# Performance work log

Measured on AMD Instinct MI355X. Metric: run time of the kernel, lower is better.

Reference implementation:

```python
import jax, jax.numpy as jnp
import numpy as np

DK = 128
B, S = 16, 2048

def setup_inputs() -> dict:
    key = jax.random.key(0)
    kq, kk, kv = jax.random.split(key, 3)
    q = jax.random.normal(kq, (B, S, DK), dtype=jnp.float32)
    k = jax.random.normal(kk, (B, S, DK), dtype=jnp.float32)
    v = jax.random.normal(kv, (B, S, DK), dtype=jnp.float32)
    return {"q": q, "k": k, "v": v}

def reference(q, k, v):
    # scores: [B, S, S]
    scale = 1.0 / jnp.sqrt(jnp.float32(DK))
    scores = jnp.einsum("bqd,bkd->bqk", q, k) * scale
    probs = jax.nn.softmax(scores, axis=-1)
    # dropout is identity in eval mode (training=None)
    return jnp.einsum("bqk,bkd->bqd", probs, v)
```

## Files before the change

### kernel.cpp

```cpp
#include <hip/hip_runtime.h>
#include <hip/hip_bf16.h>

#define BATCH 16
#define SEQ   2048
#define DK    128
#define NT    (SEQ / 2 / 32)
#define SC2   0.12751744f
#define THRL2 11.541560f

typedef __attribute__((ext_vector_type(8))) short short8v;
typedef __attribute__((ext_vector_type(4))) float float4v;

typedef const __attribute__((address_space(1))) unsigned int* gas_t;
typedef __attribute__((address_space(3))) unsigned int* las_t;

__device__ inline void gl_lds16(const void* g, void* l) {
    __builtin_amdgcn_global_load_lds((gas_t)g, (las_t)l, 16, 0, 0);
}

__device__ inline short f2bf(float f) {
    __hip_bfloat16 h = __float2bfloat16(f);
    unsigned short u;
    __builtin_memcpy(&u, &h, sizeof(u));
    return (short)u;
}

__device__ inline unsigned cvt_pk_bf16(float a, float b) {
    unsigned r;
    asm("v_cvt_pk_bf16_f32 %0, %1, %2" : "=v"(r) : "v"(a), "v"(b));
    return r;
}

__global__ __launch_bounds__(256)
void conv_k_kernel(const float* __restrict__ k, short* __restrict__ kb)
{
    size_t i = ((size_t)blockIdx.x * 256 + threadIdx.x) * 8;
    float4 a = *reinterpret_cast<const float4*>(k + i);
    float4 b = *reinterpret_cast<const float4*>(k + i + 4);
    short8v t;
    t[0] = f2bf(a.x * SC2); t[1] = f2bf(a.y * SC2); t[2] = f2bf(a.z * SC2); t[3] = f2bf(a.w * SC2);
    t[4] = f2bf(b.x * SC2); t[5] = f2bf(b.y * SC2); t[6] = f2bf(b.z * SC2); t[7] = f2bf(b.w * SC2);
    *reinterpret_cast<short8v*>(kb + i) = t;
}

__global__ __launch_bounds__(256)
void transpose_v_kernel(const float* __restrict__ v, short* __restrict__ vt)
{
    __shared__ float tile[32][33];
    const int tx = threadIdx.x & 31;
    const int ty = threadIdx.x >> 5;
    const int b  = blockIdx.z;
    const int s0 = blockIdx.x * 32;
    const int d0 = blockIdx.y * 32;

    const float* vb = v + ((size_t)b * SEQ + s0) * DK + d0;
#pragma unroll
    for (int i = 0; i < 4; ++i) {
        int r = ty + 8 * i;
        tile[r][tx] = vb[(size_t)r * DK + tx];
    }
    __syncthreads();

    const int s   = s0 + tx;
    const int kvl = s & 31;
    const int pos = (((kvl >> 2) & 3) << 3) | (((kvl >> 4) & 1) << 2) | (kvl & 3);
    const size_t col = (size_t)(s & ~31) | pos;

    short* vtb = vt + ((size_t)b * DK + d0) * SEQ;
#pragma unroll
    for (int i = 0; i < 4; ++i) {
        int r = ty + 8 * i;
        vtb[(size_t)r * SEQ + col] = f2bf(tile[tx][r]);
    }
}

__global__ __launch_bounds__(512)
void attn_fwd_v5(const float* __restrict__ q,
                 const short* __restrict__ kb,
                 const short* __restrict__ vt,
                 float* __restrict__ out)
{
    __shared__ __align__(16) char lds[65536];

    const int tid  = threadIdx.x;
    const int lane = tid & 63;
    const int wave = tid >> 6;
    const int qt   = wave & 3;
    const int h    = wave >> 2;
    const int b    = blockIdx.y;
    const int q0   = blockIdx.x * 64 + qt * 16;

    const int row  = lane & 15;
    const int grp  = lane >> 4;
    const int kswz = (row & 7) << 4;
    const int vswz = ((row >> 1) & 3) << 4;

    const float* qb = q + ((size_t)b * SEQ + q0) * DK;
    short8v qf[4];
#pragma unroll
    for (int c = 0; c < 4; ++c) {
        const float* p = qb + row * DK + c * 32 + grp * 8;
        float4 x = *reinterpret_cast<const float4*>(p);
        float4 y = *reinterpret_cast<const float4*>(p + 4);
        union { unsigned u[4]; short8v v; } pk;
        pk.u[0] = cvt_pk_bf16(x.x, x.y);
        pk.u[1] = cvt_pk_bf16(x.z, x.w);
        pk.u[2] = cvt_pk_bf16(y.x, y.y);
        pk.u[3] = cvt_pk_bf16(y.z, y.w);
        qf[c] = pk.v;
    }

    const char* kB = (const char*)(kb + (size_t)b * SEQ * DK);
    const char* vB = (const char*)(vt + (size_t)b * DK * SEQ);

    const char* src0[4];
    int         sstr[4];
    int         dsto[4];
#pragma unroll
    for (int i = 0; i < 4; ++i) {
        const int c = wave * 4 + i;
        if (c < 16) {
            const int hh = c >> 3, cc = c & 7;
            const int kr = 4 * cc + (lane >> 4);
            src0[i] = kB + (size_t)(hh * 1024 + kr) * 256
                         + (((lane & 15) << 4) ^ ((kr & 7) << 4));
            sstr[i] = 32 * 256;
            dsto[i] = hh * 8192 + cc * 1024;
        } else {
            const int hh = (c >> 3) & 1, cc = c & 7;
            const int vd = 16 * cc + (lane >> 2);
            src0[i] = vB + (size_t)vd * 4096 + hh * 2048
                         + (((lane & 3) << 4) ^ (((lane >> 3) & 3) << 4));
            sstr[i] = 32 * 2;
            dsto[i] = 16384 + hh * 8192 + cc * 1024;
        }
    }

    float m_run = -1e30f;
    float l_run = 0.0f;
    float4v o[8];
#pragma unroll
    for (int i = 0; i < 8; ++i) { o[i][0] = 0.f; o[i][1] = 0.f; o[i][2] = 0.f; o[i][3] = 0.f; }

    auto STAGE = [&](int bufsel, int t) {
        char* base = lds + bufsel * 32768;
#pragma unroll
        for (int i = 0; i < 4; ++i)
            gl_lds16(src0[i] + (size_t)t * sstr[i], base + dsto[i]);
    };

    STAGE(0, 0);
    __syncthreads();

    int buf = 0;
    for (int t = 0; t < NT; ++t) {
        if (t + 1 < NT) STAGE(buf ^ 1, t + 1);

        const char* Kl = lds + buf * 32768 + h * 8192;
        const char* Vl = lds + buf * 32768 + 16384 + h * 8192;

        float4v s[2];
        __builtin_amdgcn_s_setprio(1);
#pragma unroll
        for (int sub = 0; sub < 2; ++sub) {
            s[sub][0] = 0.f; s[sub][1] = 0.f; s[sub][2] = 0.f; s[sub][3] = 0.f;
            const char* kr = Kl + (sub * 16 + row) * 256;
#pragma unroll
            for (int c = 0; c < 4; ++c) {
                short8v kf = *reinterpret_cast<const short8v*>(kr + (((c << 6) | (grp << 4)) ^ kswz));
                s[sub] = __builtin_amdgcn_mfma_f32_16x16x32_bf16(kf, qf[c], s[sub], 0, 0, 0);
            }
        }
        __builtin_amdgcn_s_setprio(0);

        float mx = fmaxf(fmaxf(fmaxf(s[0][0], s[0][1]), fmaxf(s[0][2], s[0][3])),
                         fmaxf(fmaxf(s[1][0], s[1][1]), fmaxf(s[1][2], s[1][3])));
        mx = fmaxf(mx, __shfl_xor(mx, 16));
        mx = fmaxf(mx, __shfl_xor(mx, 32));

        if (!__all(mx <= m_run + THRL2)) {
            const float mnew  = fmaxf(m_run, mx);
            const float alpha = exp2f(m_run - mnew);
            l_run *= alpha;
            m_run = mnew;
            float aq[4];
#pragma unroll
            for (int r = 0; r < 4; ++r) aq[r] = __shfl(alpha, grp * 4 + r);
#pragma unroll
            for (int dblk = 0; dblk < 8; ++dblk)
#pragma unroll
                for (int r = 0; r < 4; ++r) o[dblk][r] *= aq[r];
        }

        float tsum = 0.f;
#pragma unroll
        for (int sub = 0; sub < 2; ++sub)
#pragma unroll
            for (int r = 0; r < 4; ++r) {
                const float e = exp2f(s[sub][r] - m_run);
                s[sub][r] = e;
                tsum += e;
            }
        tsum += __shfl_xor(tsum, 16);
        tsum += __shfl_xor(tsum, 32);
        l_run += tsum;

        union { unsigned u[4]; short8v v; } pk;
        pk.u[0] = cvt_pk_bf16(s[0][0], s[0][1]);
        pk.u[1] = cvt_pk_bf16(s[0][2], s[0][3]);
        pk.u[2] = cvt_pk_bf16(s[1][0], s[1][1]);
        pk.u[3] = cvt_pk_bf16(s[1][2], s[1][3]);
        const short8v pf = pk.v;

        __builtin_amdgcn_s_setprio(1);
#pragma unroll
        for (int dblk = 0; dblk < 8; ++dblk) {
            const short8v vf = *reinterpret_cast<const short8v*>(
                Vl + (dblk * 16 + row) * 64 + ((grp << 4) ^ vswz));
            o[dblk] = __builtin_amdgcn_mfma_f32_16x16x32_bf16(pf, vf, o[dblk], 0, 0, 0);
        }
        __builtin_amdgcn_s_setprio(0);

        __syncthreads();
        buf ^= 1;
    }

    float* smO = (float*)lds;
    float* smM = (float*)(lds + 33792);
    float* smL = (float*)(lds + 34048);

    if (h == 1) {
        smM[qt * 16 + row] = m_run;
        smL[qt * 16 + row] = l_run;
#pragma unroll
        for (int dblk = 0; dblk < 8; ++dblk)
#pragma unroll
            for (int r = 0; r < 4; ++r)
                smO[(qt * 16 + grp * 4 + r) * 132 + dblk * 16 + row] = o[dblk][r];
    }
    __syncthreads();
    if (h == 0) {
        const float m1 = smM[qt * 16 + row];
        const float l1 = smL[qt * 16 + row];
        const float mf = fmaxf(m_run, m1);
        const float a0 = exp2f(m_run - mf);
        const float a1 = exp2f(m1 - mf);
        const float lf = l_run * a0 + l1 * a1;
        const float li = 1.0f / lf;

        float a0q[4], a1q[4], liq[4];
#pragma unroll
        for (int r = 0; r < 4; ++r) {
            a0q[r] = __shfl(a0, grp * 4 + r);
            a1q[r] = __shfl(a1, grp * 4 + r);
            liq[r] = __shfl(li, grp * 4 + r);
        }

        float* ob = out + ((size_t)b * SEQ + q0) * DK;
#pragma unroll
        for (int dblk = 0; dblk < 8; ++dblk)
#pragma unroll
            for (int r = 0; r < 4; ++r) {
                float val = (o[dblk][r] * a0q[r]
                             + smO[(qt * 16 + grp * 4 + r) * 132 + dblk * 16 + row] * a1q[r]) * liq[r];
                ob[(size_t)(grp * 4 + r) * DK + dblk * 16 + row] = val;
            }
    }
}

__global__ __launch_bounds__(256)
void attn_fwd_slow(const float* __restrict__ q,
                   const float* __restrict__ k,
                   const float* __restrict__ v,
                   float* __restrict__ out)
{
    const int lane = threadIdx.x & 63;
    const int wave = threadIdx.x >> 6;
    const int b    = blockIdx.y;
    const int q0   = blockIdx.x * 64 + wave * 16;
    const int row = lane & 15;
    const int grp = lane >> 4;

    const float* qb = q + ((size_t)b * SEQ + q0) * DK;
    const float* kbp = k + (size_t)b * SEQ * DK;
    const float* vbp = v + (size_t)b * SEQ * DK;

    short8v qf[4];
#pragma unroll
    for (int c = 0; c < 4; ++c) {
        const float* p = qb + row * DK + c * 32 + grp * 8;
        float4 x = *reinterpret_cast<const float4*>(p);
        float4 y = *reinterpret_cast<const float4*>(p + 4);
        short8v t;
        t[0] = f2bf(x.x); t[1] = f2bf(x.y); t[2] = f2bf(x.z); t[3] = f2bf(x.w);
        t[4] = f2bf(y.x); t[5] = f2bf(y.y); t[6] = f2bf(y.z); t[7] = f2bf(y.w);
        qf[c] = t;
    }

    float m_run = -1e30f, l_run = 0.0f;
    float4v o[8];
#pragma unroll
    for (int i = 0; i < 8; ++i) { o[i][0]=0.f; o[i][1]=0.f; o[i][2]=0.f; o[i][3]=0.f; }
    const float scale = 0.08838834764831845f;

    for (int kv0 = 0; kv0 < SEQ; kv0 += 16) {
        short8v kf[4];
        const float* kp0 = kbp + (size_t)(kv0 + row) * DK + grp * 8;
#pragma unroll
        for (int c = 0; c < 4; ++c) {
            const float* p = kp0 + c * 32;
            float4 x = *reinterpret_cast<const float4*>(p);
            float4 y = *reinterpret_cast<const float4*>(p + 4);
            short8v t;
            t[0] = f2bf(x.x); t[1] = f2bf(x.y); t[2] = f2bf(x.z); t[3] = f2bf(x.w);
            t[4] = f2bf(y.x); t[5] = f2bf(y.y); t[6] = f2bf(y.z); t[7] = f2bf(y.w);
            kf[c] = t;
        }
        short8v vf[8];
#pragma unroll
        for (int dblk = 0; dblk < 8; ++dblk) {
            const float* p = vbp + (size_t)(kv0 + 4 * grp) * DK + dblk * 16 + row;
            short b0 = f2bf(p[0]);
            short b1 = f2bf(p[DK]);
            short b2 = f2bf(p[2 * DK]);
            short b3 = f2bf(p[3 * DK]);
            short8v t;
            t[0]=b0; t[1]=b1; t[2]=b2; t[3]=b3; t[4]=b0; t[5]=b1; t[6]=b2; t[7]=b3;
            vf[dblk] = t;
        }
        float4v s; s[0]=0.f; s[1]=0.f; s[2]=0.f; s[3]=0.f;
#pragma unroll
        for (int c = 0; c < 4; ++c)
            s = __builtin_amdgcn_mfma_f32_16x16x32_bf16(kf[c], qf[c], s, 0, 0, 0);

        float sv[4]; float tmax = -1e30f;
#pragma unroll
        for (int r = 0; r < 4; ++r) { sv[r] = s[r] * scale; tmax = fmaxf(tmax, sv[r]); }
        tmax = fmaxf(tmax, __shfl_xor(tmax, 16));
        tmax = fmaxf(tmax, __shfl_xor(tmax, 32));
        const float mnew = fmaxf(m_run, tmax);
        float pr[4]; float tsum = 0.f;
#pragma unroll
        for (int r = 0; r < 4; ++r) { pr[r] = __expf(sv[r] - mnew); tsum += pr[r]; }
        tsum += __shfl_xor(tsum, 16);
        tsum += __shfl_xor(tsum, 32);
        const float alpha = __expf(m_run - mnew);
        l_run = l_run * alpha + tsum;
        m_run = mnew;
        float aq[4];
#pragma unroll
        for (int r = 0; r < 4; ++r) aq[r] = __shfl(alpha, grp * 4 + r);
#pragma unroll
        for (int dblk = 0; dblk < 8; ++dblk)
#pragma unroll
            for (int r = 0; r < 4; ++r) o[dblk][r] *= aq[r];

        short8v pf;
        pf[0]=f2bf(pr[0]); pf[1]=f2bf(pr[1]); pf[2]=f2bf(pr[2]); pf[3]=f2bf(pr[3]);
        pf[4]=0; pf[5]=0; pf[6]=0; pf[7]=0;
#pragma unroll
        for (int dblk = 0; dblk < 8; ++dblk)
            o[dblk] = __builtin_amdgcn_mfma_f32_16x16x32_bf16(pf, vf[dblk], o[dblk], 0, 0, 0);
    }

    const float linv = 1.0f / l_run;
    float li[4];
#pragma unroll
    for (int r = 0; r < 4; ++r) li[r] = __shfl(linv, grp * 4 + r);
    float* ob = out + ((size_t)b * SEQ + q0) * DK;
#pragma unroll
    for (int dblk = 0; dblk < 8; ++dblk)
#pragma unroll
        for (int r = 0; r < 4; ++r)
            ob[(size_t)(grp * 4 + r) * DK + dblk * 16 + row] = o[dblk][r] * li[r];
}

extern "C" void kernel_launch(void* const* d_in, const int* in_sizes, int n_in,
                              void* d_out, int out_size, void* d_ws, size_t ws_size,
                              hipStream_t stream) {
    const float* q = (const float*)d_in[0];
    const float* k = (const float*)d_in[1];
    const float* v = (const float*)d_in[2];
    float* out = (float*)d_out;

    const size_t kb_bytes = (size_t)BATCH * SEQ * DK * sizeof(short);
    const size_t need = 2 * kb_bytes;

    if (ws_size >= need) {
        short* kb = (short*)d_ws;
        short* vt = (short*)((char*)d_ws + kb_bytes);
        hipLaunchKernelGGL(conv_k_kernel, dim3(2048), dim3(256), 0, stream, k, kb);
        hipLaunchKernelGGL(transpose_v_kernel, dim3(SEQ / 32, DK / 32, BATCH), dim3(256), 0, stream, v, vt);
        hipLaunchKernelGGL(attn_fwd_v5, dim3(SEQ / 64, BATCH), dim3(512), 0, stream, q, kb, vt, out);
    } else {
        hipLaunchKernelGGL(attn_fwd_slow, dim3(SEQ / 64, BATCH), dim3(256), 0, stream, q, k, v, out);
    }
}
```

Baseline: 74.02 us.

## Switch attention to 32x32x16 MFMA tiles with 128-query blocks and 64-key steps

Reworks the attention kernel so each wave handles 32 query rows with 32x32x16 bf16 MFMAs instead of 16x16x32. The KV step per iteration grows from 32 to 64 keys per half, and LDS double buffers grow to 128KB. The V transpose permutation and the LDS swizzles are changed to match the new fragment layouts. The aim is more work per loaded K/V tile and fewer instructions and syncs per FLOP, at the cost of half as many blocks (256) and much higher register and LDS pressure per block.

New measurement: 64.62 us. 12.7% less time.

```diff
diff --git a/kernel.cpp b/kernel.cpp
--- a/kernel.cpp
+++ b/kernel.cpp
@@ -4,12 +4,13 @@
 #define BATCH 16
 #define SEQ   2048
 #define DK    128
-#define NT    (SEQ / 2 / 32)
+#define NT    16
 #define SC2   0.12751744f
 #define THRL2 11.541560f
 
-typedef __attribute__((ext_vector_type(8))) short short8v;
-typedef __attribute__((ext_vector_type(4))) float float4v;
+typedef __attribute__((ext_vector_type(8)))  short short8v;
+typedef __attribute__((ext_vector_type(4)))  float float4v;
+typedef __attribute__((ext_vector_type(16))) float float16v;
 
 typedef const __attribute__((address_space(1))) unsigned int* gas_t;
 typedef __attribute__((address_space(3))) unsigned int* las_t;
@@ -62,9 +63,9 @@
     __syncthreads();
 
     const int s   = s0 + tx;
-    const int kvl = s & 31;
-    const int pos = (((kvl >> 2) & 3) << 3) | (((kvl >> 4) & 1) << 2) | (kvl & 3);
-    const size_t col = (size_t)(s & ~31) | pos;
+    const int kvl = s & 15;
+    const int pos = (((kvl >> 2) & 1) << 3) | (((kvl >> 3) & 1) << 2) | (kvl & 3);
+    const size_t col = (size_t)(s & ~15) | pos;
 
     short* vtb = vt + ((size_t)b * DK + d0) * SEQ;
 #pragma unroll
@@ -74,13 +75,13 @@
     }
 }
 
-__global__ __launch_bounds__(512)
-void attn_fwd_v5(const float* __restrict__ q,
+__global__ __launch_bounds__(512, 2)
+void attn_fwd_v6(const float* __restrict__ q,
                  const short* __restrict__ kb,
                  const short* __restrict__ vt,
                  float* __restrict__ out)
 {
-    __shared__ __align__(16) char lds[65536];
+    __shared__ __align__(16) char lds[131072];
 
     const int tid  = threadIdx.x;
     const int lane = tid & 63;
@@ -88,65 +89,65 @@
     const int qt   = wave & 3;
     const int h    = wave >> 2;
     const int b    = blockIdx.y;
-    const int q0   = blockIdx.x * 64 + qt * 16;
-
-    const int row  = lane & 15;
-    const int grp  = lane >> 4;
-    const int kswz = (row & 7) << 4;
-    const int vswz = ((row >> 1) & 3) << 4;
-
-    const float* qb = q + ((size_t)b * SEQ + q0) * DK;
-    short8v qf[4];
-#pragma unroll
-    for (int c = 0; c < 4; ++c) {
-        const float* p = qb + row * DK + c * 32 + grp * 8;
-        float4 x = *reinterpret_cast<const float4*>(p);
-        float4 y = *reinterpret_cast<const float4*>(p + 4);
+    const int q0   = blockIdx.x * 128 + qt * 32;
+
+    const int l31 = lane & 31;
+    const int hi  = lane >> 5;
+
+    const float* qrow = q + ((size_t)b * SEQ + q0 + l31) * DK + hi * 8;
+    short8v qf[8];
+#pragma unroll
+    for (int s = 0; s < 8; ++s) {
+        float4 x = *reinterpret_cast<const float4*>(qrow + s * 16);
+        float4 y = *reinterpret_cast<const float4*>(qrow + s * 16 + 4);
         union { unsigned u[4]; short8v v; } pk;
         pk.u[0] = cvt_pk_bf16(x.x, x.y);
         pk.u[1] = cvt_pk_bf16(x.z, x.w);
         pk.u[2] = cvt_pk_bf16(y.x, y.y);
         pk.u[3] = cvt_pk_bf16(y.z, y.w);
-        qf[c] = pk.v;
+        qf[s] = pk.v;
     }
 
     const char* kB = (const char*)(kb + (size_t)b * SEQ * DK);
     const char* vB = (const char*)(vt + (size_t)b * DK * SEQ);
-
-    const char* src0[4];
-    int         sstr[4];
-    int         dsto[4];
-#pragma unroll
-    for (int i = 0; i < 4; ++i) {
-        const int c = wave * 4 + i;
-        if (c < 16) {
-            const int hh = c >> 3, cc = c & 7;
-            const int kr = 4 * cc + (lane >> 4);
-            src0[i] = kB + (size_t)(hh * 1024 + kr) * 256
-                         + (((lane & 15) << 4) ^ ((kr & 7) << 4));
-            sstr[i] = 32 * 256;
-            dsto[i] = hh * 8192 + cc * 1024;
-        } else {
-            const int hh = (c >> 3) & 1, cc = c & 7;
-            const int vd = 16 * cc + (lane >> 2);
-            src0[i] = vB + (size_t)vd * 4096 + hh * 2048
-                         + (((lane & 3) << 4) ^ (((lane >> 3) & 3) << 4));
-            sstr[i] = 32 * 2;
-            dsto[i] = 16384 + hh * 8192 + cc * 1024;
-        }
+    const int hkv = h * 1024;
+
+    const char* src[8];
+    int dstoff[8];
+    long sstep;
+    if (qt < 2) {
+#pragma unroll
+        for (int i = 0; i < 8; ++i) {
+            const int kr = qt * 32 + i * 4 + (lane >> 4);
+            src[i] = kB + (size_t)(hkv + kr) * 256 + (((lane & 15) ^ (kr & 15)) << 4);
+            dstoff[i] = h * 32768 + qt * 8192 + i * 1024;
+        }
+        sstep = 64 * 256;
+    } else {
+#pragma unroll
+        for (int i = 0; i < 8; ++i) {
+            const int R  = (qt - 2) * 32 + i * 4 + (lane >> 4);
+            const int wx = (lane & 15) ^ (R & 15);
+            const int d  = 2 * R + (wx >> 3);
+            src[i] = vB + (size_t)d * (SEQ * 2) + (size_t)hkv * 2 + ((wx & 7) << 4);
+            dstoff[i] = h * 32768 + 16384 + (qt - 2) * 8192 + i * 1024;
+        }
+        sstep = 64 * 2;
     }
 
     float m_run = -1e30f;
     float l_run = 0.0f;
-    float4v o[8];
-#pragma unroll
-    for (int i = 0; i < 8; ++i) { o[i][0] = 0.f; o[i][1] = 0.f; o[i][2] = 0.f; o[i][3] = 0.f; }
+    float16v o[4];
+#pragma unroll
+    for (int dblk = 0; dblk < 4; ++dblk)
+#pragma unroll
+        for (int i = 0; i < 16; ++i) o[dblk][i] = 0.f;
 
     auto STAGE = [&](int bufsel, int t) {
-        char* base = lds + bufsel * 32768;
-#pragma unroll
-        for (int i = 0; i < 4; ++i)
-            gl_lds16(src0[i] + (size_t)t * sstr[i], base + dsto[i]);
+        char* base = lds + bufsel * 65536;
+#pragma unroll
+        for (int i = 0; i < 8; ++i)
+            gl_lds16(src[i] + (size_t)t * sstep, base + dstoff[i]);
     };
 
     STAGE(0, 0);
@@ -156,26 +157,29 @@
     for (int t = 0; t < NT; ++t) {
         if (t + 1 < NT) STAGE(buf ^ 1, t + 1);
 
-        const char* Kl = lds + buf * 32768 + h * 8192;
-        const char* Vl = lds + buf * 32768 + 16384 + h * 8192;
-
-        float4v s[2];
+        const char* Kl = lds + buf * 65536 + h * 32768;
+        const char* Vl = Kl + 16384;
+        const char* ka = Kl + l31 * 256;
+
+        float16v sa[2];
+#pragma unroll
+        for (int i = 0; i < 16; ++i) { sa[0][i] = 0.f; sa[1][i] = 0.f; }
         __builtin_amdgcn_s_setprio(1);
 #pragma unroll
-        for (int sub = 0; sub < 2; ++sub) {
-            s[sub][0] = 0.f; s[sub][1] = 0.f; s[sub][2] = 0.f; s[sub][3] = 0.f;
-            const char* kr = Kl + (sub * 16 + row) * 256;
-#pragma unroll
-            for (int c = 0; c < 4; ++c) {
-                short8v kf = *reinterpret_cast<const short8v*>(kr + (((c << 6) | (grp << 4)) ^ kswz));
-                s[sub] = __builtin_amdgcn_mfma_f32_16x16x32_bf16(kf, qf[c], s[sub], 0, 0, 0);
-            }
+        for (int s = 0; s < 8; ++s) {
+            const int un = ((2 * s + hi) ^ (l31 & 15)) << 4;
+            short8v kf0 = *reinterpret_cast<const short8v*>(ka + un);
+            short8v kf1 = *reinterpret_cast<const short8v*>(ka + 8192 + un);
+            sa[0] = __builtin_amdgcn_mfma_f32_32x32x16_bf16(kf0, qf[s], sa[0], 0, 0, 0);
+            sa[1] = __builtin_amdgcn_mfma_f32_32x32x16_bf16(kf1, qf[s], sa[1], 0, 0, 0);
         }
         __builtin_amdgcn_s_setprio(0);
 
-        float mx = fmaxf(fmaxf(fmaxf(s[0][0], s[0][1]), fmaxf(s[0][2], s[0][3])),
-                         fmaxf(fmaxf(s[1][0], s[1][1]), fmaxf(s[1][2], s[1][3])));
-        mx = fmaxf(mx, __shfl_xor(mx, 16));
+        float mx = sa[0][0];
+#pragma unroll
+        for (int i = 1; i < 16; ++i) mx = fmaxf(mx, sa[0][i]);
+#pragma unroll
+        for (int i = 0; i < 16; ++i) mx = fmaxf(mx, sa[1][i]);
         mx = fmaxf(mx, __shfl_xor(mx, 32));
 
         if (!__all(mx <= m_run + THRL2)) {
@@ -183,41 +187,52 @@
             const float alpha = exp2f(m_run - mnew);
             l_run *= alpha;
             m_run = mnew;
-            float aq[4];
-#pragma unroll
-            for (int r = 0; r < 4; ++r) aq[r] = __shfl(alpha, grp * 4 + r);
-#pragma unroll
-            for (int dblk = 0; dblk < 8; ++dblk)
-#pragma unroll
-                for (int r = 0; r < 4; ++r) o[dblk][r] *= aq[r];
-        }
-
-        float tsum = 0.f;
+            float aq[16];
+#pragma unroll
+            for (int reg = 0; reg < 16; ++reg)
+                aq[reg] = __shfl(alpha, (reg & 3) + 8 * (reg >> 2) + 4 * hi);
+#pragma unroll
+            for (int dblk = 0; dblk < 4; ++dblk)
+#pragma unroll
+                for (int reg = 0; reg < 16; ++reg) o[dblk][reg] *= aq[reg];
+        }
+
+        float ts = 0.f;
 #pragma unroll
         for (int sub = 0; sub < 2; ++sub)
 #pragma unroll
-            for (int r = 0; r < 4; ++r) {
-                const float e = exp2f(s[sub][r] - m_run);
-                s[sub][r] = e;
-                tsum += e;
+            for (int i = 0; i < 16; ++i) {
+                const float e = exp2f(sa[sub][i] - m_run);
+                sa[sub][i] = e;
+                ts += e;
             }
-        tsum += __shfl_xor(tsum, 16);
-        tsum += __shfl_xor(tsum, 32);
-        l_run += tsum;
-
-        union { unsigned u[4]; short8v v; } pk;
-        pk.u[0] = cvt_pk_bf16(s[0][0], s[0][1]);
-        pk.u[1] = cvt_pk_bf16(s[0][2], s[0][3]);
-        pk.u[2] = cvt_pk_bf16(s[1][0], s[1][1]);
-        pk.u[3] = cvt_pk_bf16(s[1][2], s[1][3]);
-        const short8v pf = pk.v;
+        ts += __shfl_xor(ts, 32);
+        l_run += ts;
+
+        short8v pf[4];
+#pragma unroll
+        for (int g = 0; g < 4; ++g) {
+            const int sub = g >> 1, r0 = (g & 1) * 8;
+            union { unsigned u[4]; short8v v; } pk;
+            pk.u[0] = cvt_pk_bf16(sa[sub][r0 + 0], sa[sub][r0 + 1]);
+            pk.u[1] = cvt_pk_bf16(sa[sub][r0 + 2], sa[sub][r0 + 3]);
+            pk.u[2] = cvt_pk_bf16(sa[sub][r0 + 4], sa[sub][r0 + 5]);
+            pk.u[3] = cvt_pk_bf16(sa[sub][r0 + 6], sa[sub][r0 + 7]);
+            pf[g] = pk.v;
+        }
 
         __builtin_amdgcn_s_setprio(1);
 #pragma unroll
-        for (int dblk = 0; dblk < 8; ++dblk) {
-            const short8v vf = *reinterpret_cast<const short8v*>(
-                Vl + (dblk * 16 + row) * 64 + ((grp << 4) ^ vswz));
-            o[dblk] = __builtin_amdgcn_mfma_f32_16x16x32_bf16(pf, vf, o[dblk], 0, 0, 0);
+        for (int dblk = 0; dblk < 4; ++dblk) {
+            const int R  = dblk * 16 + (l31 >> 1);
+            const char* vr = Vl + R * 256;
+            const int dh = (l31 & 1) << 3;
+#pragma unroll
+            for (int g = 0; g < 4; ++g) {
+                const int w = ((dh | (2 * g + hi)) ^ (R & 15)) << 4;
+                short8v vf = *reinterpret_cast<const short8v*>(vr + w);
+                o[dblk] = __builtin_amdgcn_mfma_f32_32x32x16_bf16(pf[g], vf, o[dblk], 0, 0, 0);
+            }
         }
         __builtin_amdgcn_s_setprio(0);
 
@@ -226,44 +241,47 @@
     }
 
     float* smO = (float*)lds;
-    float* smM = (float*)(lds + 33792);
-    float* smL = (float*)(lds + 34048);
+    float* smM = (float*)(lds + 65536);
+    float* smL = (float*)(lds + 66048);
 
     if (h == 1) {
-        smM[qt * 16 + row] = m_run;
-        smL[qt * 16 + row] = l_run;
-#pragma unroll
-        for (int dblk = 0; dblk < 8; ++dblk)
-#pragma unroll
-            for (int r = 0; r < 4; ++r)
-                smO[(qt * 16 + grp * 4 + r) * 132 + dblk * 16 + row] = o[dblk][r];
+        if (hi == 0) { smM[qt * 32 + l31] = m_run; smL[qt * 32 + l31] = l_run; }
+#pragma unroll
+        for (int dblk = 0; dblk < 4; ++dblk)
+#pragma unroll
+            for (int reg = 0; reg < 16; ++reg) {
+                const int qp = (reg & 3) + 8 * (reg >> 2) + 4 * hi;
+                smO[(qt * 32 + qp) * 128 + dblk * 32 + l31] = o[dblk][reg];
+            }
     }
     __syncthreads();
     if (h == 0) {
-        const float m1 = smM[qt * 16 + row];
-        const float l1 = smL[qt * 16 + row];
+        const float m1 = smM[qt * 32 + l31];
+        const float l1 = smL[qt * 32 + l31];
         const float mf = fmaxf(m_run, m1);
         const float a0 = exp2f(m_run - mf);
         const float a1 = exp2f(m1 - mf);
-        const float lf = l_run * a0 + l1 * a1;
-        const float li = 1.0f / lf;
-
-        float a0q[4], a1q[4], liq[4];
-#pragma unroll
-        for (int r = 0; r < 4; ++r) {
-            a0q[r] = __shfl(a0, grp * 4 + r);
-            a1q[r] = __shfl(a1, grp * 4 + r);
-            liq[r] = __shfl(li, grp * 4 + r);
+        const float li = 1.0f / (l_run * a0 + l1 * a1);
+        const float w0 = a0 * li;
+        const float w1 = a1 * li;
+
+        float w0q[16], w1q[16];
+#pragma unroll
+        for (int reg = 0; reg < 16; ++reg) {
+            const int qp = (reg & 3) + 8 * (reg >> 2) + 4 * hi;
+            w0q[reg] = __shfl(w0, qp);
+            w1q[reg] = __shfl(w1, qp);
         }
 
         float* ob = out + ((size_t)b * SEQ + q0) * DK;
 #pragma unroll
-        for (int dblk = 0; dblk < 8; ++dblk)
-#pragma unroll
-            for (int r = 0; r < 4; ++r) {
-                float val = (o[dblk][r] * a0q[r]
-                             + smO[(qt * 16 + grp * 4 + r) * 132 + dblk * 16 + row] * a1q[r]) * liq[r];
-                ob[(size_t)(grp * 4 + r) * DK + dblk * 16 + row] = val;
+        for (int dblk = 0; dblk < 4; ++dblk)
+#pragma unroll
+            for (int reg = 0; reg < 16; ++reg) {
+                const int qp = (reg & 3) + 8 * (reg >> 2) + 4 * hi;
+                ob[(size_t)qp * DK + dblk * 32 + l31] =
+                    o[dblk][reg] * w0q[reg]
+                    + smO[(qt * 32 + qp) * 128 + dblk * 32 + l31] * w1q[reg];
             }
     }
 }
@@ -355,12 +373,12 @@
 #pragma unroll
             for (int r = 0; r < 4; ++r) o[dblk][r] *= aq[r];
 
-        short8v pf;
-        pf[0]=f2bf(pr[0]); pf[1]=f2bf(pr[1]); pf[2]=f2bf(pr[2]); pf[3]=f2bf(pr[3]);
-        pf[4]=0; pf[5]=0; pf[6]=0; pf[7]=0;
+        short8v pfv;
+        pfv[0]=f2bf(pr[0]); pfv[1]=f2bf(pr[1]); pfv[2]=f2bf(pr[2]); pfv[3]=f2bf(pr[3]);
+        pfv[4]=0; pfv[5]=0; pfv[6]=0; pfv[7]=0;
 #pragma unroll
         for (int dblk = 0; dblk < 8; ++dblk)
-            o[dblk] = __builtin_amdgcn_mfma_f32_16x16x32_bf16(pf, vf[dblk], o[dblk], 0, 0, 0);
+            o[dblk] = __builtin_amdgcn_mfma_f32_16x16x32_bf16(pfv, vf[dblk], o[dblk], 0, 0, 0);
     }
 
     const float linv = 1.0f / l_run;
@@ -391,7 +409,7 @@
         short* vt = (short*)((char*)d_ws + kb_bytes);
         hipLaunchKernelGGL(conv_k_kernel, dim3(2048), dim3(256), 0, stream, k, kb);
         hipLaunchKernelGGL(transpose_v_kernel, dim3(SEQ / 32, DK / 32, BATCH), dim3(256), 0, stream, v, vt);
-        hipLaunchKernelGGL(attn_fwd_v5, dim3(SEQ / 64, BATCH), dim3(512), 0, stream, q, kb, vt, out);
+        hipLaunchKernelGGL(attn_fwd_v6, dim3(SEQ / 128, BATCH), dim3(512), 0, stream, q, kb, vt, out);
     } else {
         hipLaunchKernelGGL(attn_fwd_slow, dim3(SEQ / 64, BATCH), dim3(256), 0, stream, q, k, v, out);
     }
```
